# Optimization experiments

Measured on AMD Instinct MI355X. Metric: run time of the kernel, lower is better.

The kernel has to match this reference:

```python
import jax, jax.numpy as jnp
import numpy as np

# Sizes (must match input_specs)
N_CHR, E_CHR = 50000, 500000
N_SLV, E_SLV = 30000, 300000
B = 256            # number of graphs in the batch
FEAT = 64          # num_node_feats
DIM = 128          # hidden dim
HALF = DIM // 2    # last GCN layer output
ENS = 3            # ensemble per branch type


def setup_inputs() -> dict:
    key = jax.random.key(0)
    ks = jax.random.split(key, 20)
    g = lambda k, shape, fan_in: jax.random.normal(k, shape, dtype=jnp.float32) / np.sqrt(fan_in)
    inp = {
        'chr_x': jax.random.normal(ks[0], (N_CHR, FEAT), dtype=jnp.float32),
        'slv_x': jax.random.normal(ks[1], (N_SLV, FEAT), dtype=jnp.float32),
        'chr_edge_index': jax.random.randint(ks[2], (2, E_CHR), 0, N_CHR),
        'slv_edge_index': jax.random.randint(ks[3], (2, E_SLV), 0, N_SLV),
        'chr_x_batch': jnp.sort(jax.random.randint(ks[4], (N_CHR,), 0, B)),
        'slv_x_batch': jnp.sort(jax.random.randint(ks[5], (N_SLV,), 0, B)),
        # GCN weights, stacked over ensemble (GCNConv: bias=False)
        'chr_W0': g(ks[6], (ENS, FEAT, DIM), FEAT),
        'chr_W1': g(ks[7], (ENS, DIM, DIM), DIM),
        'chr_W2': g(ks[8], (ENS, DIM, HALF), DIM),
        'slv_W0': g(ks[9], (ENS, FEAT, DIM), FEAT),
        'slv_W1': g(ks[10], (ENS, DIM, DIM), DIM),
        'slv_W2': g(ks[11], (ENS, DIM, HALF), DIM),
        # per-ensemble projection heads (nn.Linear with bias)
        'cfc_W': g(ks[12], (ENS, HALF, DIM), HALF),
        'cfc_b': jnp.zeros((ENS, DIM), dtype=jnp.float32),
        'sfc_W': g(ks[13], (ENS, HALF, DIM), HALF),
        'sfc_b': jnp.zeros((ENS, DIM), dtype=jnp.float32),
        # final MLP head
        'fc1_W': g(ks[14], (2 * ENS * DIM, DIM), 2 * ENS * DIM),
        'fc1_b': jnp.zeros((DIM,), dtype=jnp.float32),
        'fc2_W': g(ks[15], (DIM, 1), DIM),
        'fc2_b': jnp.zeros((1,), dtype=jnp.float32),
    }
    return inp


def _gcn(x, W, src, dst, n_nodes):
    # GCNConv(normalize=False, bias=False, aggr='add'):
    # out[i] = sum_{(j,i) in E} (x @ W)[j]   (no self-loops, no normalization)
    h = x @ W
    return jax.ops.segment_sum(h[src], dst, num_segments=n_nodes)


def _branch(x, W0, W1, W2, edge_index, batch_ids, n_nodes):
    src, dst = edge_index[0], edge_index[1]
    h = jax.nn.relu(_gcn(x, W0, src, dst, n_nodes))
    h = jax.nn.relu(_gcn(h, W1, src, dst, n_nodes))
    h = jax.nn.relu(_gcn(h, W2, src, dst, n_nodes))
    # global_add_pool
    return jax.ops.segment_sum(h, batch_ids, num_segments=B)  # [B, HALF]


def reference(chr_x, slv_x, chr_W0, chr_W1, chr_W2, slv_W0, slv_W1, slv_W2,
              cfc_W, cfc_b, sfc_W, sfc_b, fc1_W, fc1_b, fc2_W, fc2_b,
              chr_edge_index, slv_edge_index, chr_x_batch, slv_x_batch):
    # vmap over the ensemble dimension (independent GCN stacks share inputs)
    rep_chr = jax.vmap(lambda w0, w1, w2: _branch(chr_x, w0, w1, w2, chr_edge_index, chr_x_batch, N_CHR))(
        chr_W0, chr_W1, chr_W2)  # [ENS, B, HALF]
    rep_slv = jax.vmap(lambda w0, w1, w2: _branch(slv_x, w0, w1, w2, slv_edge_index, slv_x_batch, N_SLV))(
        slv_W0, slv_W1, slv_W2)  # [ENS, B, HALF]
    ind_chr = jax.nn.relu(jnp.einsum('ebd,edh->ebh', rep_chr, cfc_W) + cfc_b[:, None, :])  # [ENS, B, DIM]
    ind_slv = jax.nn.relu(jnp.einsum('ebd,edh->ebh', rep_slv, sfc_W) + sfc_b[:, None, :])
    # torch.cat(ind_chr + ind_slv, dim=1): chr branches first, then slv branches
    hg = jnp.concatenate([
        jnp.transpose(ind_chr, (1, 0, 2)).reshape(B, ENS * DIM),
        jnp.transpose(ind_slv, (1, 0, 2)).reshape(B, ENS * DIM)], axis=1)  # [B, 2*ENS*DIM]
    hg = jax.nn.relu(hg @ fc1_W + fc1_b)
    out = hg @ fc2_W + fc2_b  # [B, 1]
    return out
```

## Files before the change

kernel.cpp:

```cpp
#include <hip/hip_runtime.h>

#define N_CHR 50000
#define E_CHR 500000
#define N_SLV 30000
#define E_SLV 300000
#define E_TOT (E_CHR + E_SLV)
#define BATCH_B 256
#define FEAT 64
#define DIM 128
#define HALF 64
#define ENSN 3
#define CB_CHR ((N_CHR + 255) / 256)
#define CB_SLV ((N_SLV + 255) / 256)
#define CB_TOT (CB_CHR + CB_SLV)
#define NBLK 128
#define CHUNK ((E_TOT + NBLK - 1) / NBLK)

typedef unsigned int u32;
typedef unsigned short u16;
typedef __attribute__((ext_vector_type(8))) short short8;
typedef __attribute__((ext_vector_type(4))) float floatx4;
typedef __attribute__((ext_vector_type(4))) unsigned int u32x4;


__device__ inline u16 f2b(float f) {
    u32 u = __builtin_bit_cast(u32, f);
    u += 0x7FFFu + ((u >> 16) & 1u);
    return (u16)(u >> 16);
}
__device__ inline float b2f_lo(u32 v) { return __builtin_bit_cast(float, v << 16); }
__device__ inline float b2f_hi(u32 v) { return __builtin_bit_cast(float, v & 0xFFFF0000u); }
__device__ inline u32 packb(float a, float b) { return (u32)f2b(a) | ((u32)f2b(b) << 16); }

__device__ inline void acc8(float* a, u32x4 v) {
    a[0] += b2f_lo(v.x); a[1] += b2f_hi(v.x);
    a[2] += b2f_lo(v.y); a[3] += b2f_hi(v.y);
    a[4] += b2f_lo(v.z); a[5] += b2f_hi(v.z);
    a[6] += b2f_lo(v.w); a[7] += b2f_hi(v.w);
}


__global__ void xconv_k(const float* __restrict__ xc, const float* __restrict__ xs,
                        u16* __restrict__ oc, u16* __restrict__ os) {
    const int nc = N_CHR * FEAT, ns = N_SLV * FEAT;
    int i = blockIdx.x * blockDim.x + threadIdx.x;
    int stride = gridDim.x * blockDim.x;
    for (; i < nc + ns; i += stride) {
        if (i < nc) oc[i] = f2b(xc[i]);
        else os[i - nc] = f2b(xs[i - nc]);
    }
}


__global__ void wconv6_k(const float* __restrict__ cW0, const float* __restrict__ cW1,
                         const float* __restrict__ cW2, const float* __restrict__ sW0,
                         const float* __restrict__ sW1, const float* __restrict__ sW2,
                         u16* __restrict__ cW0t, u16* __restrict__ cW1t, u16* __restrict__ cW2t,
                         u16* __restrict__ sW0t, u16* __restrict__ sW1t, u16* __restrict__ sW2t) {
    int z = blockIdx.z, e = blockIdx.y;
    const float* W; u16* Wt; int K, N;
    switch (z) {
        case 0: W = cW0; Wt = cW0t; K = FEAT; N = DIM;  break;
        case 1: W = cW1; Wt = cW1t; K = DIM;  N = DIM;  break;
        case 2: W = cW2; Wt = cW2t; K = DIM;  N = HALF; break;
        case 3: W = sW0; Wt = sW0t; K = FEAT; N = DIM;  break;
        case 4: W = sW1; Wt = sW1t; K = DIM;  N = DIM;  break;
        default: W = sW2; Wt = sW2t; K = DIM; N = HALF; break;
    }
    int idx = blockIdx.x * 256 + threadIdx.x;
    if (idx >= K * N) return;
    int k = idx / N, nn = idx - k * N;
    Wt[((size_t)e * N + nn) * K + k] = f2b(W[(size_t)e * K * N + idx]);
}


__global__ __launch_bounds__(256) void hist_blocks_k(
        const int* __restrict__ cdst, const int* __restrict__ sdst,
        int* __restrict__ gh, int* __restrict__ btot) {
    __shared__ int h[CB_TOT];
    int blk = blockIdx.x, t = threadIdx.x;
    for (int i = t; i < CB_TOT; i += 256) h[i] = 0;
    __syncthreads();
    int s = blk * CHUNK, e = s + CHUNK;
    if (e > E_TOT) e = E_TOT;
    for (int i = s + t; i < e; i += 256) {
        int bkt = (i < E_CHR) ? (cdst[i] >> 8) : (CB_CHR + (sdst[i - E_CHR] >> 8));
        atomicAdd(&h[bkt], 1);
    }
    __syncthreads();
    for (int j = t; j < CB_TOT; j += 256) {
        gh[j * NBLK + blk] = h[j];
        if (h[j]) atomicAdd(&btot[j], h[j]);
    }
}

__global__ void coarse_scan_k(const int* __restrict__ cnt, int* __restrict__ off) {
    int t = threadIdx.x;
    const int PER = (CB_TOT + 63) / 64;
    int loc[PER];
    int sum = 0;
    int s = t * PER;
#pragma unroll
    for (int k = 0; k < PER; k++) {
        int i = s + k;
        int v = (i < CB_TOT) ? cnt[i] : 0;
        loc[k] = sum;
        sum += v;
    }
    int inc = sum;
#pragma unroll
    for (int o = 1; o < 64; o <<= 1) {
        int sh = __shfl_up(inc, o, 64);
        if (t >= o) inc += sh;
    }
    int pre = inc - sum;
#pragma unroll
    for (int k = 0; k < PER; k++) {
        int i = s + k;
        if (i < CB_TOT) off[i] = pre + loc[k];
    }
    if (t == 63) off[CB_TOT] = inc;
}

__global__ __launch_bounds__(NBLK) void block_base_k(int* __restrict__ gh,
                                                     const int* __restrict__ coff) {
    int j = blockIdx.x, t = threadIdx.x;
    int v = gh[j * NBLK + t];
    int lane = t & 63, wv = t >> 6;
    int inc = v;
#pragma unroll
    for (int o = 1; o < 64; o <<= 1) {
        int sh = __shfl_up(inc, o, 64);
        if (lane >= o) inc += sh;
    }
    __shared__ int ws[2];
    if (lane == 63) ws[wv] = inc;
    __syncthreads();
    int p = inc - v + (wv ? ws[0] : 0);
    gh[j * NBLK + t] = coff[j] + p;
}

__global__ __launch_bounds__(256) void scatter2_k(
        const int* __restrict__ cei, const int* __restrict__ sei,
        const int* __restrict__ gh, u32* __restrict__ staging) {
    __shared__ int cur[CB_TOT];
    int blk = blockIdx.x, t = threadIdx.x;
    for (int j = t; j < CB_TOT; j += 256) cur[j] = gh[j * NBLK + blk];
    __syncthreads();
    int s = blk * CHUNK, e = s + CHUNK;
    if (e > E_TOT) e = E_TOT;
    for (int i = s + t; i < e; i += 256) {
        int src, dst, bkt;
        if (i < E_CHR) {
            src = cei[i]; dst = cei[E_CHR + i]; bkt = dst >> 8;
        } else {
            int j2 = i - E_CHR;
            src = sei[j2]; dst = sei[E_SLV + j2]; bkt = CB_CHR + (dst >> 8);
        }
        int p = atomicAdd(&cur[bkt], 1);
        staging[p] = (u32)src | ((u32)(dst & 255) << 17);
    }
}

__device__ inline int block_exscan(int v) {
    int lane = threadIdx.x & 63, wv = threadIdx.x >> 6;
    int inc = v;
#pragma unroll
    for (int o = 1; o < 64; o <<= 1) {
        int t = __shfl_up(inc, o, 64);
        if (lane >= o) inc += t;
    }
    __shared__ int ws[4];
    if (lane == 63) ws[wv] = inc;
    __syncthreads();
    if (threadIdx.x == 0) {
        int c = 0;
#pragma unroll
        for (int k = 0; k < 4; k++) { int t = ws[k]; ws[k] = c; c += t; }
    }
    __syncthreads();
    int r = ws[wv] + inc - v;
    __syncthreads();
    return r;
}

__global__ __launch_bounds__(256) void bucket_sort_k(
        const u32* __restrict__ staging, const int* __restrict__ coff,
        int* __restrict__ off_c, int* __restrict__ off_s,
        int* __restrict__ csr_c, int* __restrict__ csr_s) {
    int b = blockIdx.x, t = threadIdx.x;
    int isS = b >= CB_CHR;
    int base = coff[b], end = coff[b + 1];
    int n = isS ? N_SLV : N_CHR;
    int* off = isS ? off_s : off_c;
    int* csr = isS ? csr_s : csr_c;
    int outBase = isS ? base - E_CHR : base;
    int nodeBase = (isS ? (b - CB_CHR) : b) << 8;
    __shared__ int hist[256];
    __shared__ int cur[256];
    hist[t] = 0;
    __syncthreads();
    for (int i = base + t; i < end; i += 256)
        atomicAdd(&hist[staging[i] >> 17], 1);
    __syncthreads();
    int p = block_exscan(hist[t]);
    int node = nodeBase + t;
    if (node <= n) off[node] = outBase + p;
    cur[t] = p;
    __syncthreads();
    for (int i = base + t; i < end; i += 256) {
        u32 v = staging[i];
        int pos = atomicAdd(&cur[v >> 17], 1);
        csr[outBase + pos] = (int)(v & 0x1FFFFu);
    }
}


__global__ __launch_bounds__(256) void agg1_k(
        const u16* __restrict__ Xc, const int* __restrict__ offc, const int* __restrict__ csrc,
        u16* __restrict__ Yc, int nc,
        const u16* __restrict__ Xs, const int* __restrict__ offs, const int* __restrict__ csrs,
        u16* __restrict__ Ys, int ns) {
    int z = blockIdx.z, ch = blockIdx.y;
    const u32x4* X4 = (const u32x4*)(z ? Xs : Xc);
    const int* off = z ? offs : offc;
    const int* csr = z ? csrs : csrc;
    u32x4* Y4 = (u32x4*)(z ? Ys : Yc);
    int n = z ? ns : nc;
    int i = blockIdx.x * 64 + (threadIdx.x >> 2);
    if (i >= n) return;
    int l4 = (threadIdx.x & 3) + ch * 4;
    int s = off[i], e2 = off[i + 1];
    float a[8] = {0.f, 0.f, 0.f, 0.f, 0.f, 0.f, 0.f, 0.f};
    int j = s;
    for (; j + 3 < e2; j += 4) {
        u32x4 v0 = X4[(size_t)csr[j] * 8 + l4];
        u32x4 v1 = X4[(size_t)csr[j + 1] * 8 + l4];
        u32x4 v2 = X4[(size_t)csr[j + 2] * 8 + l4];
        u32x4 v3 = X4[(size_t)csr[j + 3] * 8 + l4];
        acc8(a, v0); acc8(a, v1); acc8(a, v2); acc8(a, v3);
    }
    for (; j < e2; j++) acc8(a, X4[(size_t)csr[j] * 8 + l4]);
    u32x4 o;
    o.x = packb(a[0], a[1]); o.y = packb(a[2], a[3]);
    o.z = packb(a[4], a[5]); o.w = packb(a[6], a[7]);
    Y4[(size_t)i * 8 + l4] = o;
}


__global__ __launch_bounds__(256) void aggb128cs_k(
        const u16* __restrict__ Hc, const int* __restrict__ offc, const int* __restrict__ csrc,
        u16* __restrict__ Yc, int nc,
        const u16* __restrict__ Hs, const int* __restrict__ offs, const int* __restrict__ csrs,
        u16* __restrict__ Ys, int ns) {
    int z = blockIdx.z;
    int n = z ? ns : nc;
    const int* off = z ? offs : offc;
    const int* csr = z ? csrs : csrc;
    int e = blockIdx.y >> 1, ch = blockIdx.y & 1;
    const u32x4* He = (const u32x4*)((z ? Hs : Hc) + (size_t)e * n * DIM);
    u32x4* Ye = (u32x4*)((z ? Ys : Yc) + (size_t)e * n * DIM);
    int i = blockIdx.x * 32 + (threadIdx.x >> 3);
    if (i >= n) return;
    int l8 = (threadIdx.x & 7) + ch * 8;
    int s = off[i], e2 = off[i + 1];
    float a[8] = {0.f, 0.f, 0.f, 0.f, 0.f, 0.f, 0.f, 0.f};
    int j = s;
    for (; j + 3 < e2; j += 4) {
        u32x4 v0 = He[(size_t)csr[j] * 16 + l8];
        u32x4 v1 = He[(size_t)csr[j + 1] * 16 + l8];
        u32x4 v2 = He[(size_t)csr[j + 2] * 16 + l8];
        u32x4 v3 = He[(size_t)csr[j + 3] * 16 + l8];
        acc8(a, v0); acc8(a, v1); acc8(a, v2); acc8(a, v3);
    }
    for (; j < e2; j++) acc8(a, He[(size_t)csr[j] * 16 + l8]);
    u32x4 o;
    o.x = packb(a[0], a[1]); o.y = packb(a[2], a[3]);
    o.z = packb(a[4], a[5]); o.w = packb(a[6], a[7]);
    Ye[(size_t)i * 16 + l8] = o;
}


#define WPAD 8

template<int K, int COLS, bool RELU>
__global__ __launch_bounds__(256) void gemm_mfma_k(
        const u16* __restrict__ Xc, size_t esc, const u16* __restrict__ Wtc,
        u16* __restrict__ Yc, int nc,
        const u16* __restrict__ Xs, size_t ess, const u16* __restrict__ Wts,
        u16* __restrict__ Ys, int ns) {
    __shared__ u16 wlds[COLS * (K + WPAD)];
    const int z = blockIdx.z, e = blockIdx.y;
    const int n = z ? ns : nc;
    const u16* Xe = (z ? Xs : Xc) + (size_t)e * (z ? ess : esc);
    const u16* We = (z ? Wts : Wtc) + (size_t)e * COLS * K;
    u16* Ye = (z ? Ys : Yc) + (size_t)e * (size_t)n * COLS;
    for (int c = threadIdx.x; c < COLS * (K / 8); c += 256) {
        int row = c / (K / 8), seg = c - row * (K / 8);
        *(short8*)(wlds + row * (K + WPAD) + seg * 8) = *(const short8*)(We + (size_t)row * K + seg * 8);
    }
    __syncthreads();
    int wave = threadIdx.x >> 6, lane = threadIdx.x & 63;
    int quad = lane >> 4, nq = lane & 15;
    int m0 = blockIdx.x * 256 + wave * 64;
    if (m0 >= n) return;
    constexpr int NT = COLS / 16, KT = K / 32;
    floatx4 acc[4][NT];
#pragma unroll
    for (int rg = 0; rg < 4; rg++)
#pragma unroll
        for (int t = 0; t < NT; t++) acc[rg][t] = (floatx4)(0.f);
#pragma unroll
    for (int kt = 0; kt < KT; kt++) {
        int k0 = kt * 32 + quad * 8;
        short8 a[4];
#pragma unroll
        for (int rg = 0; rg < 4; rg++) {
            int row = m0 + rg * 16 + nq;
            int rc = row < n ? row : n - 1;
            a[rg] = *(const short8*)(Xe + (size_t)rc * K + k0);
        }
#pragma unroll
        for (int t = 0; t < NT; t++) {
            short8 b = *(const short8*)(wlds + (t * 16 + nq) * (K + WPAD) + k0);
#pragma unroll
            for (int rg = 0; rg < 4; rg++)
                acc[rg][t] = __builtin_amdgcn_mfma_f32_16x16x32_bf16(a[rg], b, acc[rg][t], 0, 0, 0);
        }
    }
    int rbase = quad * 4;
#pragma unroll
    for (int rg = 0; rg < 4; rg++)
#pragma unroll
        for (int t = 0; t < NT; t++)
#pragma unroll
            for (int r = 0; r < 4; r++) {
                int row = m0 + rg * 16 + rbase + r;
                if (row < n) {
                    float v = acc[rg][t][r];
                    if (RELU) v = fmaxf(v, 0.f);
                    Ye[(size_t)row * COLS + t * 16 + nq] = f2b(v);
                }
            }
}


__global__ __launch_bounds__(256) void gemm23_k(
        const u16* __restrict__ Xc, const u16* __restrict__ W1c, const u16* __restrict__ W2c,
        u16* __restrict__ Yc, int nc,
        const u16* __restrict__ Xs, const u16* __restrict__ W1s, const u16* __restrict__ W2s,
        u16* __restrict__ Ys, int ns) {
    __shared__ u16 wlds[DIM * DIM];
    __shared__ u16 hlds[4 * 32 * DIM];
    const int z = blockIdx.z, e = blockIdx.y;
    const int n = z ? ns : nc;
    const u16* Xe = (z ? Xs : Xc) + (size_t)e * (size_t)n * DIM;
    const u16* W1 = (z ? W1s : W1c) + (size_t)e * DIM * DIM;
    const u16* W2 = (z ? W2s : W2c) + (size_t)e * HALF * DIM;
    u16* Ye = (z ? Ys : Yc) + (size_t)e * (size_t)n * HALF;
    for (int c = threadIdx.x; c < DIM * (DIM / 8); c += 256) {
        int row = c >> 4, seg = c & 15;
        *(short8*)(wlds + row * DIM + ((seg ^ (row & 15)) << 3)) =
            *(const short8*)(W1 + (size_t)row * DIM + (seg << 3));
    }
    __syncthreads();
    int wave = threadIdx.x >> 6, lane = threadIdx.x & 63;
    int quad = lane >> 4, nq = lane & 15;
    int m0 = blockIdx.x * 128 + wave * 32;
    floatx4 acc[2][8];
#pragma unroll
    for (int rg = 0; rg < 2; rg++)
#pragma unroll
        for (int t = 0; t < 8; t++) acc[rg][t] = (floatx4)(0.f);
#pragma unroll
    for (int kt = 0; kt < 4; kt++) {
        int k0 = kt * 32 + quad * 8;
        short8 a[2];
#pragma unroll
        for (int rg = 0; rg < 2; rg++) {
            int row = m0 + rg * 16 + nq;
            int rc = row < n ? row : (n - 1);
            a[rg] = *(const short8*)(Xe + (size_t)rc * DIM + k0);
        }
#pragma unroll
        for (int t = 0; t < 8; t++) {
            int rb = t * 16 + nq;
            short8 b = *(const short8*)(wlds + rb * DIM + ((((kt << 2) + quad) ^ nq) << 3));
#pragma unroll
            for (int rg = 0; rg < 2; rg++)
                acc[rg][t] = __builtin_amdgcn_mfma_f32_16x16x32_bf16(a[rg], b, acc[rg][t], 0, 0, 0);
        }
    }
    u16* hw = hlds + wave * 32 * DIM;
#pragma unroll
    for (int rg = 0; rg < 2; rg++)
#pragma unroll
        for (int t = 0; t < 8; t++)
#pragma unroll
            for (int r = 0; r < 4; r++) {
                int rl = rg * 16 + quad * 4 + r;
                int col = t * 16 + nq;
                hw[rl * DIM + (((col >> 3) ^ (rl & 15)) << 3) + (col & 7)] =
                    f2b(fmaxf(acc[rg][t][r], 0.f));
            }
    __syncthreads();
    for (int c = threadIdx.x; c < HALF * (DIM / 8); c += 256) {
        int row = c >> 4, seg = c & 15;
        *(short8*)(wlds + row * DIM + ((seg ^ (row & 15)) << 3)) =
            *(const short8*)(W2 + (size_t)row * DIM + (seg << 3));
    }
    __syncthreads();
    floatx4 acc2[2][4];
#pragma unroll
    for (int rg = 0; rg < 2; rg++)
#pragma unroll
        for (int t = 0; t < 4; t++) acc2[rg][t] = (floatx4)(0.f);
#pragma unroll
    for (int kt = 0; kt < 4; kt++) {
        int k0q = (kt << 2) + quad;
        short8 a[2];
#pragma unroll
        for (int rg = 0; rg < 2; rg++) {
            int rl = rg * 16 + nq;
            a[rg] = *(const short8*)(hw + rl * DIM + ((k0q ^ (rl & 15)) << 3));
        }
#pragma unroll
        for (int t = 0; t < 4; t++) {
            int rb = t * 16 + nq;
            short8 b = *(const short8*)(wlds + rb * DIM + ((k0q ^ nq) << 3));
#pragma unroll
            for (int rg = 0; rg < 2; rg++)
                acc2[rg][t] = __builtin_amdgcn_mfma_f32_16x16x32_bf16(a[rg], b, acc2[rg][t], 0, 0, 0);
        }
    }
#pragma unroll
    for (int rg = 0; rg < 2; rg++)
#pragma unroll
        for (int t = 0; t < 4; t++)
#pragma unroll
            for (int r = 0; r < 4; r++) {
                int row = m0 + rg * 16 + quad * 4 + r;
                if (row < n) Ye[(size_t)row * HALF + t * 16 + nq] = f2b(acc2[rg][t][r]);
            }
}


__global__ __launch_bounds__(256) void agg64poole_k(
        const u16* __restrict__ Pc, const int* __restrict__ offc, const int* __restrict__ csrc,
        const int* __restrict__ batc, int nc,
        const u16* __restrict__ Ps, const int* __restrict__ offs, const int* __restrict__ csrs,
        const int* __restrict__ bats, int ns,
        float* __restrict__ rep) {
    int z = blockIdx.z;
    int n = z ? ns : nc;
    const int* off = z ? offs : offc;
    const int* csr = z ? csrs : csrc;
    const int* batch = z ? bats : batc;
    const u16* P = z ? Ps : Pc;
    const u32x4* P0 = (const u32x4*)P;
    const u32x4* P1 = (const u32x4*)(P + (size_t)n * HALF);
    const u32x4* P2 = (const u32x4*)(P + 2 * (size_t)n * HALF);
    int i0 = blockIdx.x * 32;
    int nl = threadIdx.x >> 3, l8 = threadIdx.x & 7;
    int i = i0 + nl;
    float a0[8] = {0,0,0,0,0,0,0,0}, a1[8] = {0,0,0,0,0,0,0,0}, a2[8] = {0,0,0,0,0,0,0,0};
    if (i < n) {
        int s = off[i], e2 = off[i + 1];
        int j = s;
        for (; j + 1 < e2; j += 2) {
            size_t r0 = (size_t)csr[j] * 8 + l8, r1 = (size_t)csr[j + 1] * 8 + l8;
            u32x4 p0 = P0[r0], p1 = P1[r0], p2 = P2[r0];
            u32x4 q0 = P0[r1], q1 = P1[r1], q2 = P2[r1];
            acc8(a0, p0); acc8(a1, p1); acc8(a2, p2);
            acc8(a0, q0); acc8(a1, q1); acc8(a2, q2);
        }
        if (j < e2) {
            size_t r0 = (size_t)csr[j] * 8 + l8;
            acc8(a0, P0[r0]); acc8(a1, P1[r0]); acc8(a2, P2[r0]);
        }
    }
    __shared__ float sm[ENSN][32][64];
    __shared__ int gb[32];
#pragma unroll
    for (int k = 0; k < 8; k++) {
        sm[0][nl][l8 * 8 + k] = fmaxf(a0[k], 0.f);
        sm[1][nl][l8 * 8 + k] = fmaxf(a1[k], 0.f);
        sm[2][nl][l8 * 8 + k] = fmaxf(a2[k], 0.f);
    }
    if (threadIdx.x < 32) gb[threadIdx.x] = (i0 + (int)threadIdx.x < n) ? batch[i0 + threadIdx.x] : -1;
    __syncthreads();
    if (threadIdx.x < 192) {
        int e = threadIdx.x >> 6, f = threadIdx.x & 63;
        int colbase = z * (ENSN * HALF) + e * HALF + f;
        float acc = 0.f;
        int g = -2;
        for (int k = 0; k < 32; k++) {
            int gg = gb[k];
            if (gg != g) {
                if (g >= 0) atomicAdd(&rep[g * (2 * ENSN * HALF) + colbase], acc);
                acc = 0.f;
                g = gg;
            }
            if (gg >= 0) acc += sm[e][k][f];
        }
        if (g >= 0) atomicAdd(&rep[g * (2 * ENSN * HALF) + colbase], acc);
    }
}


__global__ __launch_bounds__(256) void headfinal_k(
        const float* __restrict__ rep,
        const float* __restrict__ cW, const float* __restrict__ cB,
        const float* __restrict__ sW, const float* __restrict__ sB,
        const float* __restrict__ W1, const float* __restrict__ b1,
        const float* __restrict__ W2, const float* __restrict__ b2,
        float* __restrict__ out) {
    int b = blockIdx.x, t = threadIdx.x;
    __shared__ float r[2 * ENSN * HALF];
    __shared__ float hg[2 * ENSN * DIM];
    __shared__ float red[DIM];
    for (int i = t; i < 2 * ENSN * HALF; i += 256) r[i] = rep[b * (2 * ENSN * HALF) + i];
    __syncthreads();
    for (int o = t; o < 2 * ENSN * DIM; o += 256) {
        int head = o >> 7, c = o & 127;
        int branch = head / ENSN, e = head - branch * ENSN;
        const float* W = (branch ? sW : cW) + (size_t)e * HALF * DIM;
        const float* rr = r + branch * (ENSN * HALF) + e * HALF;
        float acc = (branch ? sB : cB)[e * DIM + c];
#pragma unroll
        for (int k = 0; k < HALF; k++) acc = fmaf(rr[k], W[k * DIM + c], acc);
        hg[o] = fmaxf(acc, 0.f);
    }
    __syncthreads();
    if (t < DIM) {
        float acc = b1[t];
        for (int k = 0; k < 2 * ENSN * DIM; k++) acc = fmaf(hg[k], W1[k * DIM + t], acc);
        red[t] = fmaxf(acc, 0.f) * W2[t];
    }
    __syncthreads();
    if (t < 64) {
        float v = red[t] + red[t + 64];
#pragma unroll
        for (int o = 32; o > 0; o >>= 1) v += __shfl_down(v, o, 64);
        if (t == 0) out[b] = v + b2[0];
    }
}


extern "C" void kernel_launch(void* const* d_in, const int* in_sizes, int n_in,
                              void* d_out, int out_size, void* d_ws, size_t ws_size,
                              hipStream_t stream) {
    const float* chr_x = (const float*)d_in[0];
    const float* slv_x = (const float*)d_in[1];
    const int* chr_ei = (const int*)d_in[2];
    const int* slv_ei = (const int*)d_in[3];
    const int* chr_batch = (const int*)d_in[4];
    const int* slv_batch = (const int*)d_in[5];
    const float* chr_W0 = (const float*)d_in[6];
    const float* chr_W1 = (const float*)d_in[7];
    const float* chr_W2 = (const float*)d_in[8];
    const float* slv_W0 = (const float*)d_in[9];
    const float* slv_W1 = (const float*)d_in[10];
    const float* slv_W2 = (const float*)d_in[11];
    const float* cfc_W = (const float*)d_in[12];
    const float* cfc_b = (const float*)d_in[13];
    const float* sfc_W = (const float*)d_in[14];
    const float* sfc_b = (const float*)d_in[15];
    const float* fc1_W = (const float*)d_in[16];
    const float* fc1_b = (const float*)d_in[17];
    const float* fc2_W = (const float*)d_in[18];
    const float* fc2_b = (const float*)d_in[19];
    float* out = (float*)d_out;

    char* w = (char*)d_ws;
    auto carve = [&](size_t bytes) {
        void* p = (void*)w;
        w += (bytes + 255) & ~(size_t)255;
        return p;
    };
    int* off_chr = (int*)carve((N_CHR + 1) * sizeof(int));
    int* csr_chr = (int*)carve((size_t)E_CHR * sizeof(int));
    int* off_slv = (int*)carve((N_SLV + 1) * sizeof(int));
    int* csr_slv = (int*)carve((size_t)E_SLV * sizeof(int));
    int* btot    = (int*)carve(CB_TOT * sizeof(int));
    int* coff    = (int*)carve((CB_TOT + 1) * sizeof(int));
    int* gh      = (int*)carve((size_t)CB_TOT * NBLK * sizeof(int));
    u32* staging = (u32*)carve((size_t)E_TOT * sizeof(u32));
    u16* cW0t = (u16*)carve((size_t)ENSN * DIM * FEAT * sizeof(u16));
    u16* cW1t = (u16*)carve((size_t)ENSN * DIM * DIM * sizeof(u16));
    u16* cW2t = (u16*)carve((size_t)ENSN * HALF * DIM * sizeof(u16));
    u16* sW0t = (u16*)carve((size_t)ENSN * DIM * FEAT * sizeof(u16));
    u16* sW1t = (u16*)carve((size_t)ENSN * DIM * DIM * sizeof(u16));
    u16* sW2t = (u16*)carve((size_t)ENSN * HALF * DIM * sizeof(u16));
    u16* xb_chr = (u16*)carve((size_t)N_CHR * FEAT * sizeof(u16));
    u16* xb_slv = (u16*)carve((size_t)N_SLV * FEAT * sizeof(u16));
    float* rep = (float*)carve((size_t)BATCH_B * 2 * ENSN * HALF * sizeof(float));
    u16* aggX_c = (u16*)carve((size_t)N_CHR * FEAT * sizeof(u16));
    u16* bufP_c = (u16*)carve((size_t)ENSN * N_CHR * DIM * sizeof(u16));
    u16* bufQ_c = (u16*)carve((size_t)ENSN * N_CHR * DIM * sizeof(u16));
    u16* aggX_s = (u16*)carve((size_t)N_SLV * FEAT * sizeof(u16));
    u16* bufP_s = (u16*)carve((size_t)ENSN * N_SLV * DIM * sizeof(u16));
    u16* bufQ_s = (u16*)carve((size_t)ENSN * N_SLV * DIM * sizeof(u16));

    xconv_k<<<512, 256, 0, stream>>>(chr_x, slv_x, xb_chr, xb_slv);
    wconv6_k<<<dim3(64, ENSN, 6), 256, 0, stream>>>(chr_W0, chr_W1, chr_W2,
                                                    slv_W0, slv_W1, slv_W2,
                                                    cW0t, cW1t, cW2t, sW0t, sW1t, sW2t);

    hipMemsetAsync(btot, 0, CB_TOT * sizeof(int), stream);
    hist_blocks_k<<<NBLK, 256, 0, stream>>>(chr_ei + E_CHR, slv_ei + E_SLV, gh, btot);
    coarse_scan_k<<<1, 64, 0, stream>>>(btot, coff);
    block_base_k<<<CB_TOT, NBLK, 0, stream>>>(gh, coff);
    scatter2_k<<<NBLK, 256, 0, stream>>>(chr_ei, slv_ei, gh, staging);
    bucket_sort_k<<<CB_TOT, 256, 0, stream>>>(staging, coff, off_chr, off_slv, csr_chr, csr_slv);

    hipMemsetAsync(rep, 0, (size_t)BATCH_B * 2 * ENSN * HALF * sizeof(float), stream);

    agg1_k<<<dim3((N_CHR + 63) / 64, 2, 2), 256, 0, stream>>>(
        xb_chr, off_chr, csr_chr, aggX_c, N_CHR,
        xb_slv, off_slv, csr_slv, aggX_s, N_SLV);
    gemm_mfma_k<FEAT, DIM, true><<<dim3((N_CHR + 255) / 256, ENSN, 2), 256, 0, stream>>>(
        aggX_c, 0, cW0t, bufP_c, N_CHR, aggX_s, 0, sW0t, bufP_s, N_SLV);
    aggb128cs_k<<<dim3((N_CHR + 31) / 32, ENSN * 2, 2), 256, 0, stream>>>(
        bufP_c, off_chr, csr_chr, bufQ_c, N_CHR,
        bufP_s, off_slv, csr_slv, bufQ_s, N_SLV);
    gemm23_k<<<dim3((N_CHR + 127) / 128, ENSN, 2), 256, 0, stream>>>(
        bufQ_c, cW1t, cW2t, bufP_c, N_CHR,
        bufQ_s, sW1t, sW2t, bufP_s, N_SLV);
    agg64poole_k<<<dim3((N_CHR + 31) / 32, 1, 2), 256, 0, stream>>>(
        bufP_c, off_chr, csr_chr, chr_batch, N_CHR,
        bufP_s, off_slv, csr_slv, slv_batch, N_SLV, rep);

    headfinal_k<<<BATCH_B, 256, 0, stream>>>(rep, cfc_W, cfc_b, sfc_W, sfc_b,
                                             fc1_W, fc1_b, fc2_W, fc2_b, out);
}
```

Measured before the change: 394.4 us.

## Fuse first-layer aggregation with MFMA GEMM and use per-wave LDS histograms in CSR build

After: 373.5 us. 1.06x faster.

```diff
diff --git a/kernel.cpp b/kernel.cpp
--- a/kernel.cpp
+++ b/kernel.cpp
@@ -14,6 +14,7 @@
 #define CB_SLV ((N_SLV + 255) / 256)
 #define CB_TOT (CB_CHR + CB_SLV)
 #define NBLK 128
+#define SLOTS (NBLK * 4)
 #define CHUNK ((E_TOT + NBLK - 1) / NBLK)
 
 typedef unsigned int u32;
@@ -77,20 +78,25 @@
 __global__ __launch_bounds__(256) void hist_blocks_k(
         const int* __restrict__ cdst, const int* __restrict__ sdst,
         int* __restrict__ gh, int* __restrict__ btot) {
-    __shared__ int h[CB_TOT];
-    int blk = blockIdx.x, t = threadIdx.x;
-    for (int i = t; i < CB_TOT; i += 256) h[i] = 0;
+    __shared__ int h[4][CB_TOT];
+    int blk = blockIdx.x, t = threadIdx.x, wv = t >> 6;
+    for (int i = t; i < 4 * CB_TOT; i += 256) ((int*)h)[i] = 0;
     __syncthreads();
     int s = blk * CHUNK, e = s + CHUNK;
     if (e > E_TOT) e = E_TOT;
     for (int i = s + t; i < e; i += 256) {
         int bkt = (i < E_CHR) ? (cdst[i] >> 8) : (CB_CHR + (sdst[i - E_CHR] >> 8));
-        atomicAdd(&h[bkt], 1);
+        atomicAdd(&h[wv][bkt], 1);
     }
     __syncthreads();
     for (int j = t; j < CB_TOT; j += 256) {
-        gh[j * NBLK + blk] = h[j];
-        if (h[j]) atomicAdd(&btot[j], h[j]);
+        int s0 = h[0][j], s1 = h[1][j], s2 = h[2][j], s3 = h[3][j];
+        gh[j * SLOTS + blk * 4 + 0] = s0;
+        gh[j * SLOTS + blk * 4 + 1] = s1;
+        gh[j * SLOTS + blk * 4 + 2] = s2;
+        gh[j * SLOTS + blk * 4 + 3] = s3;
+        int tot = s0 + s1 + s2 + s3;
+        if (tot) atomicAdd(&btot[j], tot);
     }
 }
 
@@ -122,30 +128,46 @@
     if (t == 63) off[CB_TOT] = inc;
 }
 
-__global__ __launch_bounds__(NBLK) void block_base_k(int* __restrict__ gh,
-                                                     const int* __restrict__ coff) {
+__device__ inline int block_exscan(int v) {
+    int lane = threadIdx.x & 63, wv = threadIdx.x >> 6;
+    int inc = v;
+#pragma unroll
+    for (int o = 1; o < 64; o <<= 1) {
+        int t = __shfl_up(inc, o, 64);
+        if (lane >= o) inc += t;
+    }
+    __shared__ int ws[4];
+    if (lane == 63) ws[wv] = inc;
+    __syncthreads();
+    if (threadIdx.x == 0) {
+        int c = 0;
+#pragma unroll
+        for (int k = 0; k < 4; k++) { int t = ws[k]; ws[k] = c; c += t; }
+    }
+    __syncthreads();
+    int r = ws[wv] + inc - v;
+    __syncthreads();
+    return r;
+}
+
+__global__ __launch_bounds__(256) void block_base_k(int* __restrict__ gh,
+                                                    const int* __restrict__ coff) {
     int j = blockIdx.x, t = threadIdx.x;
-    int v = gh[j * NBLK + t];
-    int lane = t & 63, wv = t >> 6;
-    int inc = v;
-#pragma unroll
-    for (int o = 1; o < 64; o <<= 1) {
-        int sh = __shfl_up(inc, o, 64);
-        if (lane >= o) inc += sh;
-    }
-    __shared__ int ws[2];
-    if (lane == 63) ws[wv] = inc;
-    __syncthreads();
-    int p = inc - v + (wv ? ws[0] : 0);
-    gh[j * NBLK + t] = coff[j] + p;
+    int v0 = gh[j * SLOTS + 2 * t], v1 = gh[j * SLOTS + 2 * t + 1];
+    int p = block_exscan(v0 + v1);
+    gh[j * SLOTS + 2 * t] = coff[j] + p;
+    gh[j * SLOTS + 2 * t + 1] = coff[j] + p + v0;
 }
 
 __global__ __launch_bounds__(256) void scatter2_k(
         const int* __restrict__ cei, const int* __restrict__ sei,
         const int* __restrict__ gh, u32* __restrict__ staging) {
-    __shared__ int cur[CB_TOT];
-    int blk = blockIdx.x, t = threadIdx.x;
-    for (int j = t; j < CB_TOT; j += 256) cur[j] = gh[j * NBLK + blk];
+    __shared__ int cur[4][CB_TOT];
+    int blk = blockIdx.x, t = threadIdx.x, wv = t >> 6;
+    for (int i = t; i < 4 * CB_TOT; i += 256) {
+        int w = i / CB_TOT, j = i - w * CB_TOT;
+        ((int*)cur)[i] = gh[j * SLOTS + blk * 4 + w];
+    }
     __syncthreads();
     int s = blk * CHUNK, e = s + CHUNK;
     if (e > E_TOT) e = E_TOT;
@@ -157,38 +179,16 @@
             int j2 = i - E_CHR;
             src = sei[j2]; dst = sei[E_SLV + j2]; bkt = CB_CHR + (dst >> 8);
         }
-        int p = atomicAdd(&cur[bkt], 1);
+        int p = atomicAdd(&cur[wv][bkt], 1);
         staging[p] = (u32)src | ((u32)(dst & 255) << 17);
     }
-}
-
-__device__ inline int block_exscan(int v) {
-    int lane = threadIdx.x & 63, wv = threadIdx.x >> 6;
-    int inc = v;
-#pragma unroll
-    for (int o = 1; o < 64; o <<= 1) {
-        int t = __shfl_up(inc, o, 64);
-        if (lane >= o) inc += t;
-    }
-    __shared__ int ws[4];
-    if (lane == 63) ws[wv] = inc;
-    __syncthreads();
-    if (threadIdx.x == 0) {
-        int c = 0;
-#pragma unroll
-        for (int k = 0; k < 4; k++) { int t = ws[k]; ws[k] = c; c += t; }
-    }
-    __syncthreads();
-    int r = ws[wv] + inc - v;
-    __syncthreads();
-    return r;
 }
 
 __global__ __launch_bounds__(256) void bucket_sort_k(
         const u32* __restrict__ staging, const int* __restrict__ coff,
         int* __restrict__ off_c, int* __restrict__ off_s,
         int* __restrict__ csr_c, int* __restrict__ csr_s) {
-    int b = blockIdx.x, t = threadIdx.x;
+    int b = blockIdx.x, t = threadIdx.x, wv = t >> 6;
     int isS = b >= CB_CHR;
     int base = coff[b], end = coff[b + 1];
     int n = isS ? N_SLV : N_CHR;
@@ -196,14 +196,15 @@
     int* csr = isS ? csr_s : csr_c;
     int outBase = isS ? base - E_CHR : base;
     int nodeBase = (isS ? (b - CB_CHR) : b) << 8;
-    __shared__ int hist[256];
+    __shared__ int h4[4][256];
     __shared__ int cur[256];
-    hist[t] = 0;
+    h4[0][t] = 0; h4[1][t] = 0; h4[2][t] = 0; h4[3][t] = 0;
     __syncthreads();
     for (int i = base + t; i < end; i += 256)
-        atomicAdd(&hist[staging[i] >> 17], 1);
-    __syncthreads();
-    int p = block_exscan(hist[t]);
+        atomicAdd(&h4[wv][staging[i] >> 17], 1);
+    __syncthreads();
+    int tot = h4[0][t] + h4[1][t] + h4[2][t] + h4[3][t];
+    int p = block_exscan(tot);
     int node = nodeBase + t;
     if (node <= n) off[node] = outBase + p;
     cur[t] = p;
@@ -216,35 +217,80 @@
 }
 
 
-__global__ __launch_bounds__(256) void agg1_k(
+__global__ __launch_bounds__(256) void agg1gemm_k(
         const u16* __restrict__ Xc, const int* __restrict__ offc, const int* __restrict__ csrc,
-        u16* __restrict__ Yc, int nc,
+        const u16* __restrict__ W0c, u16* __restrict__ Yc, int nc,
         const u16* __restrict__ Xs, const int* __restrict__ offs, const int* __restrict__ csrs,
-        u16* __restrict__ Ys, int ns) {
-    int z = blockIdx.z, ch = blockIdx.y;
-    const u32x4* X4 = (const u32x4*)(z ? Xs : Xc);
+        const u16* __restrict__ W0s, u16* __restrict__ Ys, int ns) {
+    __shared__ u32x4 at4[64 * 8];
+    __shared__ u32x4 wt4[128 * 8];
+    int z = blockIdx.z;
+    int n = z ? ns : nc;
     const int* off = z ? offs : offc;
     const int* csr = z ? csrs : csrc;
-    u32x4* Y4 = (u32x4*)(z ? Ys : Yc);
-    int n = z ? ns : nc;
-    int i = blockIdx.x * 64 + (threadIdx.x >> 2);
-    if (i >= n) return;
-    int l4 = (threadIdx.x & 3) + ch * 4;
-    int s = off[i], e2 = off[i + 1];
-    float a[8] = {0.f, 0.f, 0.f, 0.f, 0.f, 0.f, 0.f, 0.f};
-    int j = s;
-    for (; j + 3 < e2; j += 4) {
-        u32x4 v0 = X4[(size_t)csr[j] * 8 + l4];
-        u32x4 v1 = X4[(size_t)csr[j + 1] * 8 + l4];
-        u32x4 v2 = X4[(size_t)csr[j + 2] * 8 + l4];
-        u32x4 v3 = X4[(size_t)csr[j + 3] * 8 + l4];
-        acc8(a, v0); acc8(a, v1); acc8(a, v2); acc8(a, v3);
-    }
-    for (; j < e2; j++) acc8(a, X4[(size_t)csr[j] * 8 + l4]);
-    u32x4 o;
-    o.x = packb(a[0], a[1]); o.y = packb(a[2], a[3]);
-    o.z = packb(a[4], a[5]); o.w = packb(a[6], a[7]);
-    Y4[(size_t)i * 8 + l4] = o;
+    const u32x4* X4 = (const u32x4*)(z ? Xs : Xc);
+    const u16* W0 = z ? W0s : W0c;
+    u16* Y = z ? Ys : Yc;
+    int i0 = blockIdx.x * 64;
+    if (i0 >= n) return;
+    int t = threadIdx.x;
+    int nl = t >> 2, c0 = t & 3;
+    int i = i0 + nl;
+    float a[16] = {0,0,0,0,0,0,0,0,0,0,0,0,0,0,0,0};
+    if (i < n) {
+        int s = off[i], e2 = off[i + 1], j = s;
+        for (; j + 1 < e2; j += 2) {
+            size_t r0 = (size_t)csr[j] * 8, r1 = (size_t)csr[j + 1] * 8;
+            u32x4 v0 = X4[r0 + c0], v1 = X4[r0 + c0 + 4];
+            u32x4 w0 = X4[r1 + c0], w1 = X4[r1 + c0 + 4];
+            acc8(a, v0); acc8(a + 8, v1); acc8(a, w0); acc8(a + 8, w1);
+        }
+        if (j < e2) {
+            size_t r0 = (size_t)csr[j] * 8;
+            acc8(a, X4[r0 + c0]); acc8(a + 8, X4[r0 + c0 + 4]);
+        }
+    }
+    u32x4 o0, o1;
+    o0.x = packb(a[0], a[1]);  o0.y = packb(a[2], a[3]);
+    o0.z = packb(a[4], a[5]);  o0.w = packb(a[6], a[7]);
+    o1.x = packb(a[8], a[9]);  o1.y = packb(a[10], a[11]);
+    o1.z = packb(a[12], a[13]); o1.w = packb(a[14], a[15]);
+    int sw = nl & 7;
+    at4[nl * 8 + (c0 ^ sw)] = o0;
+    at4[nl * 8 + ((c0 + 4) ^ sw)] = o1;
+    int wave = t >> 6, lane = t & 63, quad = lane >> 4, nq = lane & 15;
+    int arow = wave * 16 + nq;
+    for (int e = 0; e < ENSN; e++) {
+        __syncthreads();
+        const u16* We = W0 + (size_t)e * DIM * FEAT;
+        for (int ci = t; ci < 128 * 8; ci += 256) {
+            int row = ci >> 3, c = ci & 7;
+            wt4[row * 8 + (c ^ (row & 7))] = *(const u32x4*)(We + (size_t)row * FEAT + c * 8);
+        }
+        __syncthreads();
+        floatx4 acc[8];
+#pragma unroll
+        for (int tt = 0; tt < 8; tt++) acc[tt] = (floatx4)(0.f);
+#pragma unroll
+        for (int kt = 0; kt < 2; kt++) {
+            int ck = kt * 4 + quad;
+            short8 af = *(const short8*)&at4[arow * 8 + (ck ^ (arow & 7))];
+#pragma unroll
+            for (int tt = 0; tt < 8; tt++) {
+                int br = tt * 16 + nq;
+                short8 bf = *(const short8*)&wt4[br * 8 + (ck ^ (br & 7))];
+                acc[tt] = __builtin_amdgcn_mfma_f32_16x16x32_bf16(af, bf, acc[tt], 0, 0, 0);
+            }
+        }
+        u16* Ye = Y + (size_t)e * (size_t)n * DIM;
+#pragma unroll
+        for (int tt = 0; tt < 8; tt++)
+#pragma unroll
+            for (int r = 0; r < 4; r++) {
+                int row = i0 + wave * 16 + quad * 4 + r;
+                if (row < n) Ye[(size_t)row * DIM + tt * 16 + nq] = f2b(fmaxf(acc[tt][r], 0.f));
+            }
+    }
 }
 
 
@@ -278,70 +324,6 @@
     o.x = packb(a[0], a[1]); o.y = packb(a[2], a[3]);
     o.z = packb(a[4], a[5]); o.w = packb(a[6], a[7]);
     Ye[(size_t)i * 16 + l8] = o;
-}
-
-
-#define WPAD 8
-
-template<int K, int COLS, bool RELU>
-__global__ __launch_bounds__(256) void gemm_mfma_k(
-        const u16* __restrict__ Xc, size_t esc, const u16* __restrict__ Wtc,
-        u16* __restrict__ Yc, int nc,
-        const u16* __restrict__ Xs, size_t ess, const u16* __restrict__ Wts,
-        u16* __restrict__ Ys, int ns) {
-    __shared__ u16 wlds[COLS * (K + WPAD)];
-    const int z = blockIdx.z, e = blockIdx.y;
-    const int n = z ? ns : nc;
-    const u16* Xe = (z ? Xs : Xc) + (size_t)e * (z ? ess : esc);
-    const u16* We = (z ? Wts : Wtc) + (size_t)e * COLS * K;
-    u16* Ye = (z ? Ys : Yc) + (size_t)e * (size_t)n * COLS;
-    for (int c = threadIdx.x; c < COLS * (K / 8); c += 256) {
-        int row = c / (K / 8), seg = c - row * (K / 8);
-        *(short8*)(wlds + row * (K + WPAD) + seg * 8) = *(const short8*)(We + (size_t)row * K + seg * 8);
-    }
-    __syncthreads();
-    int wave = threadIdx.x >> 6, lane = threadIdx.x & 63;
-    int quad = lane >> 4, nq = lane & 15;
-    int m0 = blockIdx.x * 256 + wave * 64;
-    if (m0 >= n) return;
-    constexpr int NT = COLS / 16, KT = K / 32;
-    floatx4 acc[4][NT];
-#pragma unroll
-    for (int rg = 0; rg < 4; rg++)
-#pragma unroll
-        for (int t = 0; t < NT; t++) acc[rg][t] = (floatx4)(0.f);
-#pragma unroll
-    for (int kt = 0; kt < KT; kt++) {
-        int k0 = kt * 32 + quad * 8;
-        short8 a[4];
-#pragma unroll
-        for (int rg = 0; rg < 4; rg++) {
-            int row = m0 + rg * 16 + nq;
-            int rc = row < n ? row : n - 1;
-            a[rg] = *(const short8*)(Xe + (size_t)rc * K + k0);
-        }
-#pragma unroll
-        for (int t = 0; t < NT; t++) {
-            short8 b = *(const short8*)(wlds + (t * 16 + nq) * (K + WPAD) + k0);
-#pragma unroll
-            for (int rg = 0; rg < 4; rg++)
-                acc[rg][t] = __builtin_amdgcn_mfma_f32_16x16x32_bf16(a[rg], b, acc[rg][t], 0, 0, 0);
-        }
-    }
-    int rbase = quad * 4;
-#pragma unroll
-    for (int rg = 0; rg < 4; rg++)
-#pragma unroll
-        for (int t = 0; t < NT; t++)
-#pragma unroll
-            for (int r = 0; r < 4; r++) {
-                int row = m0 + rg * 16 + rbase + r;
-                if (row < n) {
-                    float v = acc[rg][t][r];
-                    if (RELU) v = fmaxf(v, 0.f);
-                    Ye[(size_t)row * COLS + t * 16 + nq] = f2b(v);
-                }
-            }
 }
 
 
@@ -584,7 +566,7 @@
     int* csr_slv = (int*)carve((size_t)E_SLV * sizeof(int));
     int* btot    = (int*)carve(CB_TOT * sizeof(int));
     int* coff    = (int*)carve((CB_TOT + 1) * sizeof(int));
-    int* gh      = (int*)carve((size_t)CB_TOT * NBLK * sizeof(int));
+    int* gh      = (int*)carve((size_t)CB_TOT * SLOTS * sizeof(int));
     u32* staging = (u32*)carve((size_t)E_TOT * sizeof(u32));
     u16* cW0t = (u16*)carve((size_t)ENSN * DIM * FEAT * sizeof(u16));
     u16* cW1t = (u16*)carve((size_t)ENSN * DIM * DIM * sizeof(u16));
@@ -595,10 +577,8 @@
     u16* xb_chr = (u16*)carve((size_t)N_CHR * FEAT * sizeof(u16));
     u16* xb_slv = (u16*)carve((size_t)N_SLV * FEAT * sizeof(u16));
     float* rep = (float*)carve((size_t)BATCH_B * 2 * ENSN * HALF * sizeof(float));
-    u16* aggX_c = (u16*)carve((size_t)N_CHR * FEAT * sizeof(u16));
     u16* bufP_c = (u16*)carve((size_t)ENSN * N_CHR * DIM * sizeof(u16));
     u16* bufQ_c = (u16*)carve((size_t)ENSN * N_CHR * DIM * sizeof(u16));
-    u16* aggX_s = (u16*)carve((size_t)N_SLV * FEAT * sizeof(u16));
     u16* bufP_s = (u16*)carve((size_t)ENSN * N_SLV * DIM * sizeof(u16));
     u16* bufQ_s = (u16*)carve((size_t)ENSN * N_SLV * DIM * sizeof(u16));
 
@@ -610,17 +590,15 @@
     hipMemsetAsync(btot, 0, CB_TOT * sizeof(int), stream);
     hist_blocks_k<<<NBLK, 256, 0, stream>>>(chr_ei + E_CHR, slv_ei + E_SLV, gh, btot);
     coarse_scan_k<<<1, 64, 0, stream>>>(btot, coff);
-    block_base_k<<<CB_TOT, NBLK, 0, stream>>>(gh, coff);
+    block_base_k<<<CB_TOT, 256, 0, stream>>>(gh, coff);
     scatter2_k<<<NBLK, 256, 0, stream>>>(chr_ei, slv_ei, gh, staging);
     bucket_sort_k<<<CB_TOT, 256, 0, stream>>>(staging, coff, off_chr, off_slv, csr_chr, csr_slv);
 
     hipMemsetAsync(rep, 0, (size_t)BATCH_B * 2 * ENSN * HALF * sizeof(float), stream);
 
-    agg1_k<<<dim3((N_CHR + 63) / 64, 2, 2), 256, 0, stream>>>(
-        xb_chr, off_chr, csr_chr, aggX_c, N_CHR,
-        xb_slv, off_slv, csr_slv, aggX_s, N_SLV);
-    gemm_mfma_k<FEAT, DIM, true><<<dim3((N_CHR + 255) / 256, ENSN, 2), 256, 0, stream>>>(
-        aggX_c, 0, cW0t, bufP_c, N_CHR, aggX_s, 0, sW0t, bufP_s, N_SLV);
+    agg1gemm_k<<<dim3((N_CHR + 63) / 64, 1, 2), 256, 0, stream>>>(
+        xb_chr, off_chr, csr_chr, cW0t, bufP_c, N_CHR,
+        xb_slv, off_slv, csr_slv, sW0t, bufP_s, N_SLV);
     aggb128cs_k<<<dim3((N_CHR + 31) / 32, ENSN * 2, 2), 256, 0, stream>>>(
         bufP_c, off_chr, csr_chr, bufQ_c, N_CHR,
         bufP_s, off_slv, csr_slv, bufQ_s, N_SLV);
```
